# Performance work log

Measured on AMD Instinct MI355X. Metric: run time of the kernel, lower is better.

Reference implementation:

```python
import jax, jax.numpy as jnp
import numpy as np

N, DIM = 8192, 128

def setup_inputs() -> dict:
    key = jax.random.key(0)
    ks = jax.random.split(key, 9)
    s = 1.0 / np.sqrt(DIM)
    return {
        "x": jax.random.normal(ks[0], (N, DIM), dtype=jnp.float32),
        "Wq": jax.random.uniform(ks[1], (DIM, DIM), jnp.float32, -s, s),
        "bq": jax.random.uniform(ks[2], (DIM,), jnp.float32, -s, s),
        "Wk": jax.random.uniform(ks[3], (DIM, DIM), jnp.float32, -s, s),
        "bk": jax.random.uniform(ks[4], (DIM,), jnp.float32, -s, s),
        "Wv": jax.random.uniform(ks[5], (DIM, DIM), jnp.float32, -s, s),
        "bv": jax.random.uniform(ks[6], (DIM,), jnp.float32, -s, s),
        "Wo": jax.random.uniform(ks[7], (DIM, DIM), jnp.float32, -s, s),
        "bo": jax.random.uniform(ks[8], (DIM,), jnp.float32, -s, s),
    }

def reference(x, Wq, bq, Wk, bk, Wv, bv, Wo, bo):
    # nn.Linear: y = x @ W.T + b
    Q = x @ Wq.T + bq                      # [N, d]
    K = x @ Wk.T + bk                      # [N, d]
    V = x @ Wv.T + bv                      # [N, d]
    scale = 1.0 / jnp.sqrt(jnp.asarray(x.shape[-1], x.dtype))
    scores = (Q @ K.T) * scale             # [N, N] — matches original O(n^2) math
    attn = jax.nn.softmax(scores, axis=-1)
    out = attn @ V                         # [N, d]
    return out @ Wo.T + bo
```

## Files before the change

### kernel.cpp

```cpp
#include <hip/hip_runtime.h>
#include <math.h>


typedef __bf16 bf16x8 __attribute__((ext_vector_type(8)));
typedef float f32x4 __attribute__((ext_vector_type(4)));
typedef unsigned int u32x4 __attribute__((ext_vector_type(4)));
typedef unsigned int u32x2 __attribute__((ext_vector_type(2)));
typedef unsigned short us16;

#define NTOK 8192
#define CHUNKS 8

static constexpr float SCALE_L2E = 0.08838834764831845f * 1.4426950408889634f;

__device__ __forceinline__ unsigned f2bf_u(float x) {
    unsigned u = __builtin_bit_cast(unsigned, x);
    return (u + 0x7FFFu + ((u >> 16) & 1u)) >> 16;
}

__device__ __forceinline__ unsigned pk_bf16(float x, float y) {
    unsigned a = __builtin_bit_cast(unsigned, x) + 0x8000u;
    unsigned b = __builtin_bit_cast(unsigned, y) + 0x8000u;
#if __has_builtin(__builtin_amdgcn_perm)
    return __builtin_amdgcn_perm(b, a, 0x07060302u);
#else
    return (a >> 16) | (b & 0xFFFF0000u);
#endif
}

__device__ __forceinline__ bf16x8 ld_frag(const us16* p) {
    u32x4 u = *reinterpret_cast<const u32x4*>(p);
    return __builtin_bit_cast(bf16x8, u);
}

__global__ __launch_bounds__(256) void cast_all(
    const float* __restrict__ x,
    const float* __restrict__ wq, const float* __restrict__ wk,
    const float* __restrict__ wv, const float* __restrict__ wo,
    us16* __restrict__ xb,
    us16* __restrict__ wqb, us16* __restrict__ wkb,
    us16* __restrict__ wvb, us16* __restrict__ wob)
{
    int b = blockIdx.x;
    const float* src; us16* dst; int off;
    if (b < 512) { src = x; dst = xb; off = b * 2048; }
    else {
        int wi = (b - 512) >> 3, sb = (b - 512) & 7;
        src = wi == 0 ? wq : wi == 1 ? wk : wi == 2 ? wv : wo;
        dst = wi == 0 ? wqb : wi == 1 ? wkb : wi == 2 ? wvb : wob;
        off = sb * 2048;
    }
    int i = off + threadIdx.x * 8;
    f32x4 a = *reinterpret_cast<const f32x4*>(src + i);
    f32x4 c = *reinterpret_cast<const f32x4*>(src + i + 4);
    u32x4 o;
    o[0] = f2bf_u(a[0]) | (f2bf_u(a[1]) << 16);
    o[1] = f2bf_u(a[2]) | (f2bf_u(a[3]) << 16);
    o[2] = f2bf_u(c[0]) | (f2bf_u(c[1]) << 16);
    o[3] = f2bf_u(c[2]) | (f2bf_u(c[3]) << 16);
    *reinterpret_cast<u32x4*>(dst + i) = o;
}

__global__ __launch_bounds__(256) void proj_qkv(
    const us16* __restrict__ xb,
    const us16* __restrict__ wqb, const float* __restrict__ bq,
    const us16* __restrict__ wkb, const float* __restrict__ bk,
    const us16* __restrict__ wvb, const float* __restrict__ bv,
    us16* __restrict__ Qb, us16* __restrict__ Kb, us16* __restrict__ Vt)
{
    int z = blockIdx.x >> 7;
    int tile = blockIdx.x & 127;
    const us16* W = z == 0 ? wqb : z == 1 ? wkb : wvb;
    const float* bias = z == 0 ? bq : z == 1 ? bk : bv;
    float osc = z == 0 ? SCALE_L2E : 1.0f;

    int w = threadIdx.x >> 6, lane = threadIdx.x & 63;
    int quad = lane >> 4, l15 = lane & 15;
    int rbase = tile * 64 + w * 16;

    bf16x8 af[4];
#pragma unroll
    for (int ks = 0; ks < 4; ++ks)
        af[ks] = ld_frag(xb + (rbase + l15) * 128 + ks * 32 + quad * 8);

    f32x4 acc[8];
#pragma unroll
    for (int nt = 0; nt < 8; ++nt) acc[nt] = f32x4{0.f, 0.f, 0.f, 0.f};

#pragma unroll
    for (int nt = 0; nt < 8; ++nt) {
#pragma unroll
        for (int ks = 0; ks < 4; ++ks) {
            bf16x8 bf = ld_frag(W + (nt * 16 + l15) * 128 + ks * 32 + quad * 8);
            acc[nt] = __builtin_amdgcn_mfma_f32_16x16x32_bf16(af[ks], bf, acc[nt], 0, 0, 0);
        }
    }

#pragma unroll
    for (int nt = 0; nt < 8; ++nt) {
        float bb = bias[nt * 16 + l15];
        if (z < 2) {
            us16* Out = z == 0 ? Qb : Kb;
#pragma unroll
            for (int r = 0; r < 4; ++r)
                Out[(rbase + quad * 4 + r) * 128 + nt * 16 + l15] =
                    (us16)f2bf_u((acc[nt][r] + bb) * osc);
        } else {
            int d = nt * 16 + l15, r0 = rbase + quad * 4;
            u32x2 pk;
            pk[0] = f2bf_u(acc[nt][0] + bb) | (f2bf_u(acc[nt][1] + bb) << 16);
            pk[1] = f2bf_u(acc[nt][2] + bb) | (f2bf_u(acc[nt][3] + bb) << 16);
            *reinterpret_cast<u32x2*>(Vt + d * NTOK + r0) = pk;
        }
    }
}

__global__ __launch_bounds__(256, 2) void attn(
    const us16* __restrict__ Qb, const us16* __restrict__ Kb,
    const us16* __restrict__ Vt,
    float* __restrict__ Opart, float* __restrict__ Lpart)
{
    __shared__ us16 ldsK[64 * 136];
    __shared__ us16 ldsV[128 * 72];
    __shared__ us16 ldsP[4][32 * 72];

    int qtile = blockIdx.x >> 3, chunk = blockIdx.x & 7;
    int tid = threadIdx.x, w = tid >> 6, lane = tid & 63;
    int quad = lane >> 4, l15 = lane & 15;
    int qb0 = qtile * 128 + w * 32;

    bf16x8 qf[2][4];
#pragma unroll
    for (int mt = 0; mt < 2; ++mt)
#pragma unroll
        for (int ks = 0; ks < 4; ++ks)
            qf[mt][ks] = ld_frag(Qb + (qb0 + mt * 16 + l15) * 128 + ks * 32 + quad * 8);

    f32x4 o[2][8];
#pragma unroll
    for (int mt = 0; mt < 2; ++mt)
#pragma unroll
        for (int dt = 0; dt < 8; ++dt) o[mt][dt] = f32x4{0.f, 0.f, 0.f, 0.f};

    f32x4 lacc[2];
    lacc[0] = f32x4{0.f, 0.f, 0.f, 0.f};
    lacc[1] = f32x4{0.f, 0.f, 0.f, 0.f};

    u32x4 onesu;
    onesu[0] = onesu[1] = onesu[2] = onesu[3] = 0x3F803F80u;
    bf16x8 ones = __builtin_bit_cast(bf16x8, onesu);

    us16* pw = &ldsP[w][0];

    for (int it = 0; it < 16; ++it) {
        int kk = chunk * 1024 + it * 64;
#pragma unroll
        for (int c = 0; c < 4; ++c) {
            int idx = tid + c * 256;
            int r = idx >> 4, cc = idx & 15;
            *reinterpret_cast<u32x4*>(ldsK + r * 136 + cc * 8) =
                *reinterpret_cast<const u32x4*>(Kb + (kk + r) * 128 + cc * 8);
        }
#pragma unroll
        for (int c = 0; c < 4; ++c) {
            int idx = tid + c * 256;
            int r = idx >> 3, cc = idx & 7;
            *reinterpret_cast<u32x4*>(ldsV + r * 72 + cc * 8) =
                *reinterpret_cast<const u32x4*>(Vt + r * NTOK + kk + cc * 8);
        }
        __syncthreads();

        f32x4 s[2][4];
#pragma unroll
        for (int mt = 0; mt < 2; ++mt)
#pragma unroll
            for (int nt = 0; nt < 4; ++nt) s[mt][nt] = f32x4{0.f, 0.f, 0.f, 0.f};

#pragma unroll
        for (int nt = 0; nt < 4; ++nt) {
#pragma unroll
            for (int ks = 0; ks < 4; ++ks) {
                bf16x8 kf = ld_frag(ldsK + (nt * 16 + l15) * 136 + ks * 32 + quad * 8);
                s[0][nt] = __builtin_amdgcn_mfma_f32_16x16x32_bf16(kf, qf[0][ks], s[0][nt], 0, 0, 0);
                s[1][nt] = __builtin_amdgcn_mfma_f32_16x16x32_bf16(kf, qf[1][ks], s[1][nt], 0, 0, 0);
            }
        }

#pragma unroll
        for (int mt = 0; mt < 2; ++mt) {
#pragma unroll
            for (int nt = 0; nt < 4; ++nt) {
                float p0 = exp2f(s[mt][nt][0]);
                float p1 = exp2f(s[mt][nt][1]);
                float p2 = exp2f(s[mt][nt][2]);
                float p3 = exp2f(s[mt][nt][3]);
                u32x2 wv;
                wv[0] = pk_bf16(p0, p1);
                wv[1] = pk_bf16(p2, p3);
                *reinterpret_cast<u32x2*>(pw + (mt * 16 + l15) * 72 + nt * 16 + quad * 4) = wv;
            }
        }

        asm volatile("s_waitcnt lgkmcnt(0)" ::: "memory");

        bf16x8 afP[2][2];
#pragma unroll
        for (int mt = 0; mt < 2; ++mt)
#pragma unroll
            for (int k2 = 0; k2 < 2; ++k2)
                afP[mt][k2] = ld_frag(pw + (mt * 16 + l15) * 72 + k2 * 32 + quad * 8);

        lacc[0] = __builtin_amdgcn_mfma_f32_16x16x32_bf16(afP[0][0], ones, lacc[0], 0, 0, 0);
        lacc[0] = __builtin_amdgcn_mfma_f32_16x16x32_bf16(afP[0][1], ones, lacc[0], 0, 0, 0);
        lacc[1] = __builtin_amdgcn_mfma_f32_16x16x32_bf16(afP[1][0], ones, lacc[1], 0, 0, 0);
        lacc[1] = __builtin_amdgcn_mfma_f32_16x16x32_bf16(afP[1][1], ones, lacc[1], 0, 0, 0);

#pragma unroll
        for (int dt = 0; dt < 8; ++dt) {
#pragma unroll
            for (int k2 = 0; k2 < 2; ++k2) {
                bf16x8 bv = ld_frag(ldsV + (dt * 16 + l15) * 72 + k2 * 32 + quad * 8);
                o[0][dt] = __builtin_amdgcn_mfma_f32_16x16x32_bf16(afP[0][k2], bv, o[0][dt], 0, 0, 0);
                o[1][dt] = __builtin_amdgcn_mfma_f32_16x16x32_bf16(afP[1][k2], bv, o[1][dt], 0, 0, 0);
            }
        }
        __syncthreads();
    }

#pragma unroll
    for (int mt = 0; mt < 2; ++mt)
#pragma unroll
        for (int dt = 0; dt < 8; ++dt)
#pragma unroll
            for (int r = 0; r < 4; ++r) {
                int row = qb0 + mt * 16 + quad * 4 + r;
                Opart[(size_t)(chunk * NTOK + row) * 128 + dt * 16 + l15] = o[mt][dt][r];
            }
    if (l15 == 0) {
#pragma unroll
        for (int mt = 0; mt < 2; ++mt)
#pragma unroll
            for (int r = 0; r < 4; ++r) {
                int row = qb0 + mt * 16 + quad * 4 + r;
                Lpart[chunk * NTOK + row] = lacc[mt][r];
            }
    }
}

__global__ __launch_bounds__(256) void combine_proj(
    const float* __restrict__ Opart, const float* __restrict__ Lpart,
    const us16* __restrict__ wob, const float* __restrict__ bo,
    float* __restrict__ out)
{
    __shared__ us16 ldsO[64 * 136];
    __shared__ float ldsL[64];

    int tile = blockIdx.x, t = threadIdx.x;
    int r0 = tile * 64;

    if (t < 64) {
        float L = 0.f;
#pragma unroll
        for (int c = 0; c < CHUNKS; ++c) L += Lpart[c * NTOK + r0 + t];
        ldsL[t] = 1.0f / L;
    }

    f32x4 acc[8];
#pragma unroll
    for (int j = 0; j < 8; ++j) acc[j] = f32x4{0.f, 0.f, 0.f, 0.f};

#pragma unroll
    for (int c = 0; c < CHUNKS; ++c) {
        const float* src = Opart + (size_t)(c * NTOK + r0) * 128;
#pragma unroll
        for (int j = 0; j < 8; ++j) {
            f32x4 v = *reinterpret_cast<const f32x4*>(src + j * 1024 + t * 4);
            acc[j] += v;
        }
    }
    __syncthreads();

#pragma unroll
    for (int j = 0; j < 8; ++j) {
        int flat = j * 1024 + t * 4;
        int row = flat >> 7, col = flat & 127;
        float sc = ldsL[row];
        u32x2 wv;
        wv[0] = pk_bf16(acc[j][0] * sc, acc[j][1] * sc);
        wv[1] = pk_bf16(acc[j][2] * sc, acc[j][3] * sc);
        *reinterpret_cast<u32x2*>(ldsO + row * 136 + col) = wv;
    }
    __syncthreads();

    int w = t >> 6, lane = t & 63;
    int quad = lane >> 4, l15 = lane & 15;
    int rloc = w * 16;

    bf16x8 af[4];
#pragma unroll
    for (int ks = 0; ks < 4; ++ks)
        af[ks] = ld_frag(ldsO + (rloc + l15) * 136 + ks * 32 + quad * 8);

    f32x4 acc2[8];
#pragma unroll
    for (int nt = 0; nt < 8; ++nt) acc2[nt] = f32x4{0.f, 0.f, 0.f, 0.f};

#pragma unroll
    for (int nt = 0; nt < 8; ++nt) {
#pragma unroll
        for (int ks = 0; ks < 4; ++ks) {
            bf16x8 bfw = ld_frag(wob + (nt * 16 + l15) * 128 + ks * 32 + quad * 8);
            acc2[nt] = __builtin_amdgcn_mfma_f32_16x16x32_bf16(af[ks], bfw, acc2[nt], 0, 0, 0);
        }
    }
#pragma unroll
    for (int nt = 0; nt < 8; ++nt) {
        float bb = bo[nt * 16 + l15];
#pragma unroll
        for (int r = 0; r < 4; ++r)
            out[(r0 + rloc + quad * 4 + r) * 128 + nt * 16 + l15] = acc2[nt][r] + bb;
    }
}

extern "C" void kernel_launch(void* const* d_in, const int* in_sizes, int n_in,
                              void* d_out, int out_size, void* d_ws, size_t ws_size,
                              hipStream_t stream)
{
    const float* x  = (const float*)d_in[0];
    const float* Wq = (const float*)d_in[1];
    const float* bq = (const float*)d_in[2];
    const float* Wk = (const float*)d_in[3];
    const float* bk = (const float*)d_in[4];
    const float* Wv = (const float*)d_in[5];
    const float* bv = (const float*)d_in[6];
    const float* Wo = (const float*)d_in[7];
    const float* bo = (const float*)d_in[8];

    char* ws = (char*)d_ws;
    const size_t MB = 1024 * 1024;
    us16* xb  = (us16*)(ws + 0 * MB);
    us16* Qb  = (us16*)(ws + 2 * MB);
    us16* Kb  = (us16*)(ws + 4 * MB);
    us16* Vt  = (us16*)(ws + 6 * MB);
    us16* wqb = (us16*)(ws + 8 * MB);
    us16* wkb = (us16*)(ws + 8 * MB + 32 * 1024);
    us16* wvb = (us16*)(ws + 8 * MB + 64 * 1024);
    us16* wob = (us16*)(ws + 8 * MB + 96 * 1024);
    float* Lp = (float*)(ws + 8 * MB + 128 * 1024);
    float* Op = (float*)(ws + 9 * MB);

    cast_all<<<544, 256, 0, stream>>>(x, Wq, Wk, Wv, Wo, xb, wqb, wkb, wvb, wob);
    proj_qkv<<<384, 256, 0, stream>>>(xb, wqb, bq, wkb, bk, wvb, bv, Qb, Kb, Vt);
    attn<<<512, 256, 0, stream>>>(Qb, Kb, Vt, Op, Lp);
    combine_proj<<<128, 256, 0, stream>>>(Op, Lp, wob, bo, (float*)d_out);
}
```

Baseline: 151.0 us.

## Rewrite attention with 32x32 MFMA, register-resident P via permlane swap, no LDS

```diff
diff --git a/kernel.cpp b/kernel.cpp
--- a/kernel.cpp
+++ b/kernel.cpp
@@ -4,6 +4,7 @@
 
 typedef __bf16 bf16x8 __attribute__((ext_vector_type(8)));
 typedef float f32x4 __attribute__((ext_vector_type(4)));
+typedef float f32x16 __attribute__((ext_vector_type(16)));
 typedef unsigned int u32x4 __attribute__((ext_vector_type(4)));
 typedef unsigned int u32x2 __attribute__((ext_vector_type(2)));
 typedef unsigned short us16;
@@ -26,6 +27,16 @@
 #else
     return (a >> 16) | (b & 0xFFFF0000u);
 #endif
+}
+
+__device__ __forceinline__ unsigned cvtpk_bf16(float x, float y) {
+    unsigned r;
+    asm("v_cvt_pk_bf16_f32 %0, %1, %2" : "=v"(r) : "v"(x), "v"(y));
+    return r;
+}
+
+__device__ __forceinline__ void plswap(unsigned& a, unsigned& b) {
+    asm("v_permlane32_swap_b32 %0, %1" : "+v"(a), "+v"(b));
 }
 
 __device__ __forceinline__ bf16x8 ld_frag(const us16* p) {
@@ -120,131 +131,97 @@
     const us16* __restrict__ Vt,
     float* __restrict__ Opart, float* __restrict__ Lpart)
 {
-    __shared__ us16 ldsK[64 * 136];
-    __shared__ us16 ldsV[128 * 72];
-    __shared__ us16 ldsP[4][32 * 72];
-
     int qtile = blockIdx.x >> 3, chunk = blockIdx.x & 7;
     int tid = threadIdx.x, w = tid >> 6, lane = tid & 63;
-    int quad = lane >> 4, l15 = lane & 15;
-    int qb0 = qtile * 128 + w * 32;
-
-    bf16x8 qf[2][4];
-#pragma unroll
-    for (int mt = 0; mt < 2; ++mt)
-#pragma unroll
-        for (int ks = 0; ks < 4; ++ks)
-            qf[mt][ks] = ld_frag(Qb + (qb0 + mt * 16 + l15) * 128 + ks * 32 + quad * 8);
-
-    f32x4 o[2][8];
-#pragma unroll
-    for (int mt = 0; mt < 2; ++mt)
-#pragma unroll
-        for (int dt = 0; dt < 8; ++dt) o[mt][dt] = f32x4{0.f, 0.f, 0.f, 0.f};
-
-    f32x4 lacc[2];
-    lacc[0] = f32x4{0.f, 0.f, 0.f, 0.f};
-    lacc[1] = f32x4{0.f, 0.f, 0.f, 0.f};
-
-    u32x4 onesu;
-    onesu[0] = onesu[1] = onesu[2] = onesu[3] = 0x3F803F80u;
-    bf16x8 ones = __builtin_bit_cast(bf16x8, onesu);
-
-    us16* pw = &ldsP[w][0];
-
-    for (int it = 0; it < 16; ++it) {
-        int kk = chunk * 1024 + it * 64;
-#pragma unroll
-        for (int c = 0; c < 4; ++c) {
-            int idx = tid + c * 256;
-            int r = idx >> 4, cc = idx & 15;
-            *reinterpret_cast<u32x4*>(ldsK + r * 136 + cc * 8) =
-                *reinterpret_cast<const u32x4*>(Kb + (kk + r) * 128 + cc * 8);
-        }
-#pragma unroll
-        for (int c = 0; c < 4; ++c) {
-            int idx = tid + c * 256;
-            int r = idx >> 3, cc = idx & 7;
-            *reinterpret_cast<u32x4*>(ldsV + r * 72 + cc * 8) =
-                *reinterpret_cast<const u32x4*>(Vt + r * NTOK + kk + cc * 8);
-        }
-        __syncthreads();
-
-        f32x4 s[2][4];
-#pragma unroll
-        for (int mt = 0; mt < 2; ++mt)
-#pragma unroll
-            for (int nt = 0; nt < 4; ++nt) s[mt][nt] = f32x4{0.f, 0.f, 0.f, 0.f};
-
-#pragma unroll
-        for (int nt = 0; nt < 4; ++nt) {
-#pragma unroll
-            for (int ks = 0; ks < 4; ++ks) {
-                bf16x8 kf = ld_frag(ldsK + (nt * 16 + l15) * 136 + ks * 32 + quad * 8);
-                s[0][nt] = __builtin_amdgcn_mfma_f32_16x16x32_bf16(kf, qf[0][ks], s[0][nt], 0, 0, 0);
-                s[1][nt] = __builtin_amdgcn_mfma_f32_16x16x32_bf16(kf, qf[1][ks], s[1][nt], 0, 0, 0);
-            }
-        }
-
-#pragma unroll
-        for (int mt = 0; mt < 2; ++mt) {
-#pragma unroll
-            for (int nt = 0; nt < 4; ++nt) {
-                float p0 = exp2f(s[mt][nt][0]);
-                float p1 = exp2f(s[mt][nt][1]);
-                float p2 = exp2f(s[mt][nt][2]);
-                float p3 = exp2f(s[mt][nt][3]);
-                u32x2 wv;
-                wv[0] = pk_bf16(p0, p1);
-                wv[1] = pk_bf16(p2, p3);
-                *reinterpret_cast<u32x2*>(pw + (mt * 16 + l15) * 72 + nt * 16 + quad * 4) = wv;
-            }
-        }
-
-        asm volatile("s_waitcnt lgkmcnt(0)" ::: "memory");
-
-        bf16x8 afP[2][2];
-#pragma unroll
-        for (int mt = 0; mt < 2; ++mt)
-#pragma unroll
-            for (int k2 = 0; k2 < 2; ++k2)
-                afP[mt][k2] = ld_frag(pw + (mt * 16 + l15) * 72 + k2 * 32 + quad * 8);
-
-        lacc[0] = __builtin_amdgcn_mfma_f32_16x16x32_bf16(afP[0][0], ones, lacc[0], 0, 0, 0);
-        lacc[0] = __builtin_amdgcn_mfma_f32_16x16x32_bf16(afP[0][1], ones, lacc[0], 0, 0, 0);
-        lacc[1] = __builtin_amdgcn_mfma_f32_16x16x32_bf16(afP[1][0], ones, lacc[1], 0, 0, 0);
-        lacc[1] = __builtin_amdgcn_mfma_f32_16x16x32_bf16(afP[1][1], ones, lacc[1], 0, 0, 0);
-
-#pragma unroll
-        for (int dt = 0; dt < 8; ++dt) {
-#pragma unroll
-            for (int k2 = 0; k2 < 2; ++k2) {
-                bf16x8 bv = ld_frag(ldsV + (dt * 16 + l15) * 72 + k2 * 32 + quad * 8);
-                o[0][dt] = __builtin_amdgcn_mfma_f32_16x16x32_bf16(afP[0][k2], bv, o[0][dt], 0, 0, 0);
-                o[1][dt] = __builtin_amdgcn_mfma_f32_16x16x32_bf16(afP[1][k2], bv, o[1][dt], 0, 0, 0);
-            }
-        }
-        __syncthreads();
-    }
-
-#pragma unroll
-    for (int mt = 0; mt < 2; ++mt)
-#pragma unroll
-        for (int dt = 0; dt < 8; ++dt)
-#pragma unroll
-            for (int r = 0; r < 4; ++r) {
-                int row = qb0 + mt * 16 + quad * 4 + r;
-                Opart[(size_t)(chunk * NTOK + row) * 128 + dt * 16 + l15] = o[mt][dt][r];
-            }
-    if (l15 == 0) {
-#pragma unroll
-        for (int mt = 0; mt < 2; ++mt)
-#pragma unroll
-            for (int r = 0; r < 4; ++r) {
-                int row = qb0 + mt * 16 + quad * 4 + r;
-                Lpart[chunk * NTOK + row] = lacc[mt][r];
-            }
-    }
+    int l31 = lane & 31, hi = lane >> 5;
+    int qrow0 = qtile * 128 + w * 32;
+    int k0 = chunk * 1024;
+
+    bf16x8 qf[8];
+#pragma unroll
+    for (int ks = 0; ks < 8; ++ks)
+        qf[ks] = ld_frag(Qb + (qrow0 + l31) * 128 + ks * 16 + hi * 8);
+
+    f32x16 o[4];
+#pragma unroll
+    for (int dt = 0; dt < 4; ++dt)
+#pragma unroll
+        for (int r = 0; r < 16; ++r) o[dt][r] = 0.f;
+
+    float ls0 = 0.f, ls1 = 0.f;
+
+    bf16x8 kf[8];
+    {
+        const us16* kbase = Kb + (size_t)(k0 + l31) * 128 + hi * 8;
+#pragma unroll
+        for (int ks = 0; ks < 8; ++ks) kf[ks] = ld_frag(kbase + ks * 16);
+    }
+
+    for (int it = 0; it < 32; ++it) {
+        int kb = k0 + it * 32;
+
+        bf16x8 vf[8];
+        {
+            const us16* vbase = Vt + (size_t)l31 * NTOK + kb + hi * 8;
+#pragma unroll
+            for (int dt = 0; dt < 4; ++dt)
+#pragma unroll
+                for (int t = 0; t < 2; ++t)
+                    vf[dt * 2 + t] = ld_frag(vbase + (size_t)dt * 32 * NTOK + t * 16);
+        }
+
+        f32x16 s;
+#pragma unroll
+        for (int r = 0; r < 16; ++r) s[r] = 0.f;
+#pragma unroll
+        for (int ks = 0; ks < 8; ++ks)
+            s = __builtin_amdgcn_mfma_f32_32x32x16_bf16(kf[ks], qf[ks], s, 0, 0, 0);
+
+        if (it < 31) {
+            const us16* kbase = Kb + (size_t)(kb + 32 + l31) * 128 + hi * 8;
+#pragma unroll
+            for (int ks = 0; ks < 8; ++ks) kf[ks] = ld_frag(kbase + ks * 16);
+        }
+
+        float p[16];
+#pragma unroll
+        for (int r = 0; r < 16; ++r) p[r] = exp2f(s[r]);
+#pragma unroll
+        for (int r = 0; r < 16; r += 2) { ls0 += p[r]; ls1 += p[r + 1]; }
+
+        unsigned u0 = cvtpk_bf16(p[0],  p[1]),  u1 = cvtpk_bf16(p[2],  p[3]);
+        unsigned u2 = cvtpk_bf16(p[4],  p[5]),  u3 = cvtpk_bf16(p[6],  p[7]);
+        unsigned u4 = cvtpk_bf16(p[8],  p[9]),  u5 = cvtpk_bf16(p[10], p[11]);
+        unsigned u6 = cvtpk_bf16(p[12], p[13]), u7 = cvtpk_bf16(p[14], p[15]);
+
+        plswap(u0, u2);
+        plswap(u1, u3);
+        plswap(u4, u6);
+        plswap(u5, u7);
+        u32x4 f0v; f0v[0] = u0; f0v[1] = u1; f0v[2] = u2; f0v[3] = u3;
+        u32x4 f1v; f1v[0] = u4; f1v[1] = u5; f1v[2] = u6; f1v[3] = u7;
+        bf16x8 pf0 = __builtin_bit_cast(bf16x8, f0v);
+        bf16x8 pf1 = __builtin_bit_cast(bf16x8, f1v);
+
+#pragma unroll
+        for (int dt = 0; dt < 4; ++dt) {
+            o[dt] = __builtin_amdgcn_mfma_f32_32x32x16_bf16(pf0, vf[dt * 2 + 0], o[dt], 0, 0, 0);
+            o[dt] = __builtin_amdgcn_mfma_f32_32x32x16_bf16(pf1, vf[dt * 2 + 1], o[dt], 0, 0, 0);
+        }
+    }
+
+#pragma unroll
+    for (int dt = 0; dt < 4; ++dt)
+#pragma unroll
+        for (int r = 0; r < 16; ++r) {
+            int m = (r & 3) + 8 * (r >> 2) + 4 * hi;
+            Opart[(size_t)(chunk * NTOK + qrow0 + m) * 128 + dt * 32 + l31] = o[dt][r];
+        }
+
+    float lsum = ls0 + ls1;
+    float lfull = lsum + __shfl_xor(lsum, 32);
+    if (lane < 32)
+        Lpart[chunk * NTOK + qrow0 + l31] = lfull;
 }
 
 __global__ __launch_bounds__(256) void combine_proj(
@@ -252,28 +229,28 @@
     const us16* __restrict__ wob, const float* __restrict__ bo,
     float* __restrict__ out)
 {
-    __shared__ us16 ldsO[64 * 136];
-    __shared__ float ldsL[64];
+    __shared__ us16 ldsO[32 * 136];
+    __shared__ float ldsL[32];
 
     int tile = blockIdx.x, t = threadIdx.x;
-    int r0 = tile * 64;
-
-    if (t < 64) {
+    int r0 = tile * 32;
+
+    if (t < 32) {
         float L = 0.f;
 #pragma unroll
         for (int c = 0; c < CHUNKS; ++c) L += Lpart[c * NTOK + r0 + t];
         ldsL[t] = 1.0f / L;
     }
 
-    f32x4 acc[8];
-#pragma unroll
-    for (int j = 0; j < 8; ++j) acc[j] = f32x4{0.f, 0.f, 0.f, 0.f};
+    f32x4 acc[4];
+#pragma unroll
+    for (int j = 0; j < 4; ++j) acc[j] = f32x4{0.f, 0.f, 0.f, 0.f};
 
 #pragma unroll
     for (int c = 0; c < CHUNKS; ++c) {
         const float* src = Opart + (size_t)(c * NTOK + r0) * 128;
 #pragma unroll
-        for (int j = 0; j < 8; ++j) {
+        for (int j = 0; j < 4; ++j) {
             f32x4 v = *reinterpret_cast<const f32x4*>(src + j * 1024 + t * 4);
             acc[j] += v;
         }
@@ -281,7 +258,7 @@
     __syncthreads();
 
 #pragma unroll
-    for (int j = 0; j < 8; ++j) {
+    for (int j = 0; j < 4; ++j) {
         int flat = j * 1024 + t * 4;
         int row = flat >> 7, col = flat & 127;
         float sc = ldsL[row];
@@ -293,32 +270,28 @@
     __syncthreads();
 
     int w = t >> 6, lane = t & 63;
-    int quad = lane >> 4, l15 = lane & 15;
-    int rloc = w * 16;
-
-    bf16x8 af[4];
-#pragma unroll
-    for (int ks = 0; ks < 4; ++ks)
-        af[ks] = ld_frag(ldsO + (rloc + l15) * 136 + ks * 32 + quad * 8);
-
-    f32x4 acc2[8];
-#pragma unroll
-    for (int nt = 0; nt < 8; ++nt) acc2[nt] = f32x4{0.f, 0.f, 0.f, 0.f};
-
-#pragma unroll
-    for (int nt = 0; nt < 8; ++nt) {
-#pragma unroll
-        for (int ks = 0; ks < 4; ++ks) {
-            bf16x8 bfw = ld_frag(wob + (nt * 16 + l15) * 128 + ks * 32 + quad * 8);
-            acc2[nt] = __builtin_amdgcn_mfma_f32_16x16x32_bf16(af[ks], bfw, acc2[nt], 0, 0, 0);
-        }
-    }
-#pragma unroll
-    for (int nt = 0; nt < 8; ++nt) {
-        float bb = bo[nt * 16 + l15];
-#pragma unroll
-        for (int r = 0; r < 4; ++r)
-            out[(r0 + rloc + quad * 4 + r) * 128 + nt * 16 + l15] = acc2[nt][r] + bb;
+    int l31 = lane & 31, hi = lane >> 5;
+
+    bf16x8 af[8];
+#pragma unroll
+    for (int ks = 0; ks < 8; ++ks)
+        af[ks] = ld_frag(ldsO + l31 * 136 + ks * 16 + hi * 8);
+
+    f32x16 acc2;
+#pragma unroll
+    for (int r = 0; r < 16; ++r) acc2[r] = 0.f;
+
+#pragma unroll
+    for (int ks = 0; ks < 8; ++ks) {
+        bf16x8 bfw = ld_frag(wob + (w * 32 + l31) * 128 + ks * 16 + hi * 8);
+        acc2 = __builtin_amdgcn_mfma_f32_32x32x16_bf16(af[ks], bfw, acc2, 0, 0, 0);
+    }
+
+    float bb = bo[w * 32 + l31];
+#pragma unroll
+    for (int r = 0; r < 16; ++r) {
+        int m = (r & 3) + 8 * (r >> 2) + 4 * hi;
+        out[(size_t)(r0 + m) * 128 + w * 32 + l31] = acc2[r] + bb;
     }
 }
 
@@ -352,5 +325,5 @@
     cast_all<<<544, 256, 0, stream>>>(x, Wq, Wk, Wv, Wo, xb, wqb, wkb, wvb, wob);
     proj_qkv<<<384, 256, 0, stream>>>(xb, wqb, bq, wkb, bk, wvb, bv, Qb, Kb, Vt);
     attn<<<512, 256, 0, stream>>>(Qb, Kb, Vt, Op, Lp);
-    combine_proj<<<128, 256, 0, stream>>>(Op, Lp, wob, bo, (float*)d_out);
-}
+    combine_proj<<<256, 256, 0, stream>>>(Op, Lp, wob, bo, (float*)d_out);
+}
```

New measurement: 215.9 us. +43.0%, slower.

## Fuse bf16 casts into projections, stage Q/K stores via LDS, halve combine tile

Applied to the files above, without the earlier changes.

```diff
diff --git a/kernel.cpp b/kernel.cpp
--- a/kernel.cpp
+++ b/kernel.cpp
@@ -4,6 +4,7 @@
 
 typedef __bf16 bf16x8 __attribute__((ext_vector_type(8)));
 typedef float f32x4 __attribute__((ext_vector_type(4)));
+typedef float f32x16 __attribute__((ext_vector_type(16)));
 typedef unsigned int u32x4 __attribute__((ext_vector_type(4)));
 typedef unsigned int u32x2 __attribute__((ext_vector_type(2)));
 typedef unsigned short us16;
@@ -33,44 +34,29 @@
     return __builtin_bit_cast(bf16x8, u);
 }
 
-__global__ __launch_bounds__(256) void cast_all(
-    const float* __restrict__ x,
-    const float* __restrict__ wq, const float* __restrict__ wk,
-    const float* __restrict__ wv, const float* __restrict__ wo,
-    us16* __restrict__ xb,
-    us16* __restrict__ wqb, us16* __restrict__ wkb,
-    us16* __restrict__ wvb, us16* __restrict__ wob)
-{
-    int b = blockIdx.x;
-    const float* src; us16* dst; int off;
-    if (b < 512) { src = x; dst = xb; off = b * 2048; }
-    else {
-        int wi = (b - 512) >> 3, sb = (b - 512) & 7;
-        src = wi == 0 ? wq : wi == 1 ? wk : wi == 2 ? wv : wo;
-        dst = wi == 0 ? wqb : wi == 1 ? wkb : wi == 2 ? wvb : wob;
-        off = sb * 2048;
-    }
-    int i = off + threadIdx.x * 8;
-    f32x4 a = *reinterpret_cast<const f32x4*>(src + i);
-    f32x4 c = *reinterpret_cast<const f32x4*>(src + i + 4);
+__device__ __forceinline__ bf16x8 cvt_frag(const float* p) {
+    f32x4 a = *reinterpret_cast<const f32x4*>(p);
+    f32x4 b = *reinterpret_cast<const f32x4*>(p + 4);
     u32x4 o;
     o[0] = f2bf_u(a[0]) | (f2bf_u(a[1]) << 16);
     o[1] = f2bf_u(a[2]) | (f2bf_u(a[3]) << 16);
-    o[2] = f2bf_u(c[0]) | (f2bf_u(c[1]) << 16);
-    o[3] = f2bf_u(c[2]) | (f2bf_u(c[3]) << 16);
-    *reinterpret_cast<u32x4*>(dst + i) = o;
+    o[2] = f2bf_u(b[0]) | (f2bf_u(b[1]) << 16);
+    o[3] = f2bf_u(b[2]) | (f2bf_u(b[3]) << 16);
+    return __builtin_bit_cast(bf16x8, o);
 }
 
 __global__ __launch_bounds__(256) void proj_qkv(
-    const us16* __restrict__ xb,
-    const us16* __restrict__ wqb, const float* __restrict__ bq,
-    const us16* __restrict__ wkb, const float* __restrict__ bk,
-    const us16* __restrict__ wvb, const float* __restrict__ bv,
+    const float* __restrict__ x,
+    const float* __restrict__ wq, const float* __restrict__ bq,
+    const float* __restrict__ wk, const float* __restrict__ bk,
+    const float* __restrict__ wv, const float* __restrict__ bv,
     us16* __restrict__ Qb, us16* __restrict__ Kb, us16* __restrict__ Vt)
 {
+    __shared__ us16 ldsT[4][16 * 136];
+
     int z = blockIdx.x >> 7;
     int tile = blockIdx.x & 127;
-    const us16* W = z == 0 ? wqb : z == 1 ? wkb : wvb;
+    const float* W = z == 0 ? wq : z == 1 ? wk : wv;
     const float* bias = z == 0 ? bq : z == 1 ? bk : bv;
     float osc = z == 0 ? SCALE_L2E : 1.0f;
 
@@ -81,7 +67,7 @@
     bf16x8 af[4];
 #pragma unroll
     for (int ks = 0; ks < 4; ++ks)
-        af[ks] = ld_frag(xb + (rbase + l15) * 128 + ks * 32 + quad * 8);
+        af[ks] = cvt_frag(x + (rbase + l15) * 128 + ks * 32 + quad * 8);
 
     f32x4 acc[8];
 #pragma unroll
@@ -91,21 +77,34 @@
     for (int nt = 0; nt < 8; ++nt) {
 #pragma unroll
         for (int ks = 0; ks < 4; ++ks) {
-            bf16x8 bf = ld_frag(W + (nt * 16 + l15) * 128 + ks * 32 + quad * 8);
+            bf16x8 bf = cvt_frag(W + (nt * 16 + l15) * 128 + ks * 32 + quad * 8);
             acc[nt] = __builtin_amdgcn_mfma_f32_16x16x32_bf16(af[ks], bf, acc[nt], 0, 0, 0);
         }
     }
 
-#pragma unroll
-    for (int nt = 0; nt < 8; ++nt) {
-        float bb = bias[nt * 16 + l15];
-        if (z < 2) {
-            us16* Out = z == 0 ? Qb : Kb;
+    if (z < 2) {
+        us16* T = &ldsT[w][0];
+        us16* Out = z == 0 ? Qb : Kb;
+#pragma unroll
+        for (int nt = 0; nt < 8; ++nt) {
+            float bb = bias[nt * 16 + l15];
 #pragma unroll
             for (int r = 0; r < 4; ++r)
-                Out[(rbase + quad * 4 + r) * 128 + nt * 16 + l15] =
+                T[(quad * 4 + r) * 136 + nt * 16 + l15] =
                     (us16)f2bf_u((acc[nt][r] + bb) * osc);
-        } else {
+        }
+        asm volatile("s_waitcnt lgkmcnt(0)" ::: "memory");
+        int row = lane >> 2, seg = lane & 3;
+        const us16* src = T + row * 136 + seg * 32;
+        us16* dst = Out + (rbase + row) * 128 + seg * 32;
+#pragma unroll
+        for (int c = 0; c < 4; ++c)
+            *reinterpret_cast<u32x4*>(dst + c * 8) =
+                *reinterpret_cast<const u32x4*>(src + c * 8);
+    } else {
+#pragma unroll
+        for (int nt = 0; nt < 8; ++nt) {
+            float bb = bias[nt * 16 + l15];
             int d = nt * 16 + l15, r0 = rbase + quad * 4;
             u32x2 pk;
             pk[0] = f2bf_u(acc[nt][0] + bb) | (f2bf_u(acc[nt][1] + bb) << 16);
@@ -249,31 +248,31 @@
 
 __global__ __launch_bounds__(256) void combine_proj(
     const float* __restrict__ Opart, const float* __restrict__ Lpart,
-    const us16* __restrict__ wob, const float* __restrict__ bo,
+    const float* __restrict__ Wo, const float* __restrict__ bo,
     float* __restrict__ out)
 {
-    __shared__ us16 ldsO[64 * 136];
-    __shared__ float ldsL[64];
+    __shared__ us16 ldsO[32 * 136];
+    __shared__ float ldsL[32];
 
     int tile = blockIdx.x, t = threadIdx.x;
-    int r0 = tile * 64;
-
-    if (t < 64) {
+    int r0 = tile * 32;
+
+    if (t < 32) {
         float L = 0.f;
 #pragma unroll
         for (int c = 0; c < CHUNKS; ++c) L += Lpart[c * NTOK + r0 + t];
         ldsL[t] = 1.0f / L;
     }
 
-    f32x4 acc[8];
-#pragma unroll
-    for (int j = 0; j < 8; ++j) acc[j] = f32x4{0.f, 0.f, 0.f, 0.f};
+    f32x4 acc[4];
+#pragma unroll
+    for (int j = 0; j < 4; ++j) acc[j] = f32x4{0.f, 0.f, 0.f, 0.f};
 
 #pragma unroll
     for (int c = 0; c < CHUNKS; ++c) {
         const float* src = Opart + (size_t)(c * NTOK + r0) * 128;
 #pragma unroll
-        for (int j = 0; j < 8; ++j) {
+        for (int j = 0; j < 4; ++j) {
             f32x4 v = *reinterpret_cast<const f32x4*>(src + j * 1024 + t * 4);
             acc[j] += v;
         }
@@ -281,7 +280,7 @@
     __syncthreads();
 
 #pragma unroll
-    for (int j = 0; j < 8; ++j) {
+    for (int j = 0; j < 4; ++j) {
         int flat = j * 1024 + t * 4;
         int row = flat >> 7, col = flat & 127;
         float sc = ldsL[row];
@@ -293,32 +292,28 @@
     __syncthreads();
 
     int w = t >> 6, lane = t & 63;
-    int quad = lane >> 4, l15 = lane & 15;
-    int rloc = w * 16;
-
-    bf16x8 af[4];
-#pragma unroll
-    for (int ks = 0; ks < 4; ++ks)
-        af[ks] = ld_frag(ldsO + (rloc + l15) * 136 + ks * 32 + quad * 8);
-
-    f32x4 acc2[8];
-#pragma unroll
-    for (int nt = 0; nt < 8; ++nt) acc2[nt] = f32x4{0.f, 0.f, 0.f, 0.f};
-
-#pragma unroll
-    for (int nt = 0; nt < 8; ++nt) {
-#pragma unroll
-        for (int ks = 0; ks < 4; ++ks) {
-            bf16x8 bfw = ld_frag(wob + (nt * 16 + l15) * 128 + ks * 32 + quad * 8);
-            acc2[nt] = __builtin_amdgcn_mfma_f32_16x16x32_bf16(af[ks], bfw, acc2[nt], 0, 0, 0);
-        }
-    }
-#pragma unroll
-    for (int nt = 0; nt < 8; ++nt) {
-        float bb = bo[nt * 16 + l15];
-#pragma unroll
-        for (int r = 0; r < 4; ++r)
-            out[(r0 + rloc + quad * 4 + r) * 128 + nt * 16 + l15] = acc2[nt][r] + bb;
+    int l31 = lane & 31, hi = lane >> 5;
+
+    bf16x8 af[8];
+#pragma unroll
+    for (int ks = 0; ks < 8; ++ks)
+        af[ks] = ld_frag(ldsO + l31 * 136 + ks * 16 + hi * 8);
+
+    f32x16 acc2;
+#pragma unroll
+    for (int r = 0; r < 16; ++r) acc2[r] = 0.f;
+
+#pragma unroll
+    for (int ks = 0; ks < 8; ++ks) {
+        bf16x8 bfw = cvt_frag(Wo + (w * 32 + l31) * 128 + ks * 16 + hi * 8);
+        acc2 = __builtin_amdgcn_mfma_f32_32x32x16_bf16(af[ks], bfw, acc2, 0, 0, 0);
+    }
+
+    float bb = bo[w * 32 + l31];
+#pragma unroll
+    for (int r = 0; r < 16; ++r) {
+        int m = (r & 3) + 8 * (r >> 2) + 4 * hi;
+        out[(size_t)(r0 + m) * 128 + w * 32 + l31] = acc2[r] + bb;
     }
 }
 
@@ -338,19 +333,13 @@
 
     char* ws = (char*)d_ws;
     const size_t MB = 1024 * 1024;
-    us16* xb  = (us16*)(ws + 0 * MB);
-    us16* Qb  = (us16*)(ws + 2 * MB);
-    us16* Kb  = (us16*)(ws + 4 * MB);
-    us16* Vt  = (us16*)(ws + 6 * MB);
-    us16* wqb = (us16*)(ws + 8 * MB);
-    us16* wkb = (us16*)(ws + 8 * MB + 32 * 1024);
-    us16* wvb = (us16*)(ws + 8 * MB + 64 * 1024);
-    us16* wob = (us16*)(ws + 8 * MB + 96 * 1024);
-    float* Lp = (float*)(ws + 8 * MB + 128 * 1024);
-    float* Op = (float*)(ws + 9 * MB);
-
-    cast_all<<<544, 256, 0, stream>>>(x, Wq, Wk, Wv, Wo, xb, wqb, wkb, wvb, wob);
-    proj_qkv<<<384, 256, 0, stream>>>(xb, wqb, bq, wkb, bk, wvb, bv, Qb, Kb, Vt);
+    us16* Qb  = (us16*)(ws + 0 * MB);
+    us16* Kb  = (us16*)(ws + 2 * MB);
+    us16* Vt  = (us16*)(ws + 4 * MB);
+    float* Lp = (float*)(ws + 6 * MB);
+    float* Op = (float*)(ws + 7 * MB);
+
+    proj_qkv<<<384, 256, 0, stream>>>(x, Wq, bq, Wk, bk, Wv, bv, Qb, Kb, Vt);
     attn<<<512, 256, 0, stream>>>(Qb, Kb, Vt, Op, Lp);
-    combine_proj<<<128, 256, 0, stream>>>(Op, Lp, wob, bo, (float*)d_out);
-}
+    combine_proj<<<256, 256, 0, stream>>>(Op, Lp, Wo, bo, (float*)d_out);
+}
```

Result: no change. 153.0 us (+1.4%).
